# Performance work log

Measured on AMD Instinct MI355X. Metric: run time of the kernel, lower is better.

The kernel has to match this reference:

```python
import jax, jax.numpy as jnp
import numpy as np

B, L, H, O, N = 64, 2048, 128, 128, 256  # batch, window, num_states, num_actions, dynamics state dim


def setup_inputs() -> dict:
    key = jax.random.key(0)
    ks = jax.random.split(key, 12)
    # LRU-style stable init: |lambda| in (r_min, r_max)
    u1 = jax.random.uniform(ks[0], (N,))
    u2 = jax.random.uniform(ks[1], (N,))
    r_min, r_max = 0.4, 0.99
    nu_log = jnp.log(-0.5 * jnp.log(u1 * (r_max**2 - r_min**2) + r_min**2))
    theta_log = jnp.log(u2 * 2.0 * jnp.pi)
    lam_abs2 = jnp.exp(-2.0 * jnp.exp(nu_log))
    gamma_log = 0.5 * jnp.log(1.0 - lam_abs2)  # gamma normalization
    return {
        "state": jax.random.normal(ks[2], (B, H), jnp.float32),
        "dynamics_input_time_window": jax.random.normal(ks[3], (B, L, H), jnp.float32),
        "dynamics_disturbance_time_window": jax.random.normal(ks[4], (B, L, H), jnp.float32),
        "nu_log": nu_log.astype(jnp.float32),
        "theta_log": theta_log.astype(jnp.float32),
        "gamma_log": gamma_log.astype(jnp.float32),
        "B_re": jax.random.normal(ks[5], (N, H), jnp.float32) / np.sqrt(2 * H),
        "B_im": jax.random.normal(ks[6], (N, H), jnp.float32) / np.sqrt(2 * H),
        "C_re": jax.random.normal(ks[7], (O, N), jnp.float32) / np.sqrt(N),
        "C_im": jax.random.normal(ks[8], (O, N), jnp.float32) / np.sqrt(N),
        "D": jax.random.normal(ks[9], (O, H), jnp.float32) / np.sqrt(H),
    }


def _ssm_scan(u, nu_log, theta_log, gamma_log, B_re, B_im, C_re, C_im, D):
    # u: [B, L, H] real. Diagonal complex LRU: x_t = lam * x_{t-1} + gamma*B u_t; y = Re(C x) + D u
    lam = jnp.exp(-jnp.exp(nu_log) + 1j * jnp.exp(theta_log))           # [N]
    Bmat = (B_re + 1j * B_im) * jnp.exp(gamma_log)[:, None]              # [N, H]
    Bu = jnp.einsum("blh,nh->bln", u.astype(jnp.complex64), Bmat)       # [B, L, N]
    lam_seq = jnp.broadcast_to(lam, Bu.shape)

    def comb(e1, e2):
        a1, b1 = e1
        a2, b2 = e2
        return a1 * a2, a2 * b1 + b2

    _, x = jax.lax.associative_scan(comb, (lam_seq, Bu), axis=1)        # [B, L, N]
    y = jnp.einsum("bln,on->blo", x, C_re + 1j * C_im).real
    y = y + jnp.einsum("blh,oh->blo", u, D)
    return y


def reference(state, dynamics_input_time_window, dynamics_disturbance_time_window,
              nu_log, theta_log, gamma_log, B_re, B_im, C_re, C_im, D):
    # 3-dim branch of Actor.forward: run SSM over the disturbance window, take last step
    y = _ssm_scan(dynamics_disturbance_time_window, nu_log, theta_log, gamma_log,
                  B_re, B_im, C_re, C_im, D)                             # [B, L, O]
    action = y[:, -1, :]                                                 # [B, O]
    return action
```

## Files before the change

kernel.cpp:

```cpp
#include <hip/hip_runtime.h>
#include <hip/hip_bf16.h>

#define B_ 64
#define L_ 2048
#define H_ 128
#define O_ 128
#define N_ 256
#define TC_ 256
#define NCHUNK_ 8
#define NSTRIP_ 16

using f32x4 = __attribute__((ext_vector_type(4))) float;
using s16x8 = __attribute__((ext_vector_type(8))) short;
using i32x4 = __attribute__((ext_vector_type(4))) int;

__device__ __forceinline__ int pack_bf16(float a, float b) {
    return (int)((__float_as_uint(a) >> 16) | (__float_as_uint(b) & 0xffff0000u));
}

__global__ void prep_kernel(const float* __restrict__ nu_log, const float* __restrict__ theta_log,
                            const float* __restrict__ gamma_log, const float* __restrict__ B_re,
                            const float* __restrict__ B_im, unsigned short* __restrict__ B2T,
                            float2* __restrict__ lamj, float2* __restrict__ lam16t,
                            float2* __restrict__ lamC) {
    if (blockIdx.x < 64) {
        #pragma unroll
        for (int i = 0; i < 4; ++i) {
            int idx = blockIdx.x * 1024 + i * 256 + threadIdx.x;
            int col = idx >> 7;
            int h = idx & 127;
            int n = col & (N_ - 1);
            float g = expf(gamma_log[n]);
            float v = (col < N_ ? B_re[n * H_ + h] : B_im[n * H_ + h]) * g;
            unsigned ub = __float_as_uint(v);
            B2T[idx] = (unsigned short)((ub + 0x7fffu + ((ub >> 16) & 1u)) >> 16);
        }
    } else {
        int n = threadIdx.x;
        double lnr = -(double)expf(nu_log[n]);
        double th = (double)expf(theta_log[n]);
        double r = exp(lnr);
        double sn, cs;
        sincos(th, &sn, &cs);
        double lre = r * cs, lim = r * sn;
        double pre = 1.0, pim = 0.0;
        for (int k = 0; k < 16; ++k) {
            lamj[n * 16 + 15 - k] = make_float2((float)pre, (float)pim);
            double t1 = pre * lre - pim * lim;
            double t2 = pre * lim + pim * lre;
            pre = t1; pim = t2;
        }
        lam16t[n] = make_float2((float)pre, (float)pim);
        double wre = pre, wim = pim;
        for (int i = 0; i < 4; ++i) {
            double t1 = wre * wre - wim * wim;
            double t2 = 2.0 * wre * wim;
            wre = t1; wim = t2;
        }
        double are = 1.0, aim = 0.0;
        for (int cc = 7; cc >= 0; --cc) {
            lamC[cc * N_ + n] = make_float2((float)are, (float)aim);
            double t1 = are * wre - aim * wim;
            double t2 = are * wim + aim * wre;
            are = t1; aim = t2;
        }
    }
}

__global__ __launch_bounds__(256, 2)
void scan_kernel(const float* __restrict__ u, const unsigned short* __restrict__ B2T,
                 const float2* __restrict__ lamj, const float2* __restrict__ lam16t,
                 const float2* __restrict__ lamC, float* __restrict__ X) {
    const int b = blockIdx.x >> 3;
    const int c = blockIdx.x & 7;
    const int wave = (threadIdx.x >> 6) & 3;
    const int lane = threadIdx.x & 63;
    const int m = lane & 15;
    const int q = lane >> 4;

    s16x8 bf[4][2][4];
    float2 wl[4][4];
    float2 l16[4];

    #pragma unroll
    for (int p = 0; p < 4; ++p) {
        const int n = wave * 64 + p * 16 + m;
        #pragma unroll
        for (int part = 0; part < 2; ++part) {
            const unsigned short* rp = B2T + (size_t)(part * N_ + n) * H_ + q * 8;
            #pragma unroll
            for (int sl = 0; sl < 4; ++sl)
                bf[p][part][sl] = *(const s16x8*)(rp + sl * 32);
        }
        #pragma unroll
        for (int r = 0; r < 4; ++r) wl[p][r] = lamj[n * 16 + q * 4 + r];
        l16[p] = lam16t[n];
    }

    float2 zr[4], zi[4];
    #pragma unroll
    for (int p = 0; p < 4; ++p) {
        zr[p] = make_float2(0.f, 0.f);
        zi[p] = make_float2(0.f, 0.f);
    }

    const float* ub = u + ((size_t)b * L_ + (size_t)c * TC_) * H_;

    #pragma unroll 1
    for (int s = 0; s < NSTRIP_; ++s) {
        const float* up = ub + (s * 16 + m) * H_ + q * 8;
        float4 ua[8];
        #pragma unroll
        for (int sl = 0; sl < 4; ++sl) {
            ua[2 * sl]     = *(const float4*)(up + sl * 32);
            ua[2 * sl + 1] = *(const float4*)(up + sl * 32 + 4);
        }
        s16x8 afr[4];
        #pragma unroll
        for (int sl = 0; sl < 4; ++sl) {
            i32x4 w;
            w[0] = pack_bf16(ua[2 * sl].x, ua[2 * sl].y);
            w[1] = pack_bf16(ua[2 * sl].z, ua[2 * sl].w);
            w[2] = pack_bf16(ua[2 * sl + 1].x, ua[2 * sl + 1].y);
            w[3] = pack_bf16(ua[2 * sl + 1].z, ua[2 * sl + 1].w);
            afr[sl] = __builtin_bit_cast(s16x8, w);
        }
        #pragma unroll
        for (int p = 0; p < 4; ++p) {
            float2 a = zr[p];
            zr[p].x = l16[p].x * a.x - l16[p].y * a.y;
            zr[p].y = l16[p].x * a.y + l16[p].y * a.x;
            float2 bb = zi[p];
            zi[p].x = l16[p].x * bb.x - l16[p].y * bb.y;
            zi[p].y = l16[p].x * bb.y + l16[p].y * bb.x;
        }
        #pragma unroll
        for (int p = 0; p < 4; ++p) {
            f32x4 acc = {0.f, 0.f, 0.f, 0.f};
            #pragma unroll
            for (int sl = 0; sl < 4; ++sl)
                acc = __builtin_amdgcn_mfma_f32_16x16x32_bf16(afr[sl], bf[p][0][sl], acc, 0, 0, 0);
            #pragma unroll
            for (int r = 0; r < 4; ++r) {
                zr[p].x += wl[p][r].x * acc[r];
                zr[p].y += wl[p][r].y * acc[r];
            }
            f32x4 acc2 = {0.f, 0.f, 0.f, 0.f};
            #pragma unroll
            for (int sl = 0; sl < 4; ++sl)
                acc2 = __builtin_amdgcn_mfma_f32_16x16x32_bf16(afr[sl], bf[p][1][sl], acc2, 0, 0, 0);
            #pragma unroll
            for (int r = 0; r < 4; ++r) {
                zi[p].x += wl[p][r].x * acc2[r];
                zi[p].y += wl[p][r].y * acc2[r];
            }
        }
    }

    #pragma unroll
    for (int p = 0; p < 4; ++p) {
        zr[p].x += __shfl_xor(zr[p].x, 16); zr[p].x += __shfl_xor(zr[p].x, 32);
        zr[p].y += __shfl_xor(zr[p].y, 16); zr[p].y += __shfl_xor(zr[p].y, 32);
        zi[p].x += __shfl_xor(zi[p].x, 16); zi[p].x += __shfl_xor(zi[p].x, 32);
        zi[p].y += __shfl_xor(zi[p].y, 16); zi[p].y += __shfl_xor(zi[p].y, 32);
    }

    if (lane < 16) {
        #pragma unroll
        for (int p = 0; p < 4; ++p) {
            const int n = wave * 64 + p * 16 + m;
            float2 lc = lamC[c * N_ + n];
            float prr = lc.x * zr[p].x - lc.y * zr[p].y;
            float pri = lc.x * zr[p].y + lc.y * zr[p].x;
            float pir = lc.x * zi[p].x - lc.y * zi[p].y;
            float pii = lc.x * zi[p].y + lc.y * zi[p].x;
            atomicAdd(&X[(size_t)(b * N_ + n) * 2 + 0], prr - pii);
            atomicAdd(&X[(size_t)(b * N_ + n) * 2 + 1], pri + pir);
        }
    }
}

__global__ void out_kernel(const float* __restrict__ X, const float* __restrict__ C_re,
                           const float* __restrict__ C_im, const float* __restrict__ Dm,
                           const float* __restrict__ u, float* __restrict__ out) {
    __shared__ float xre[N_], xim[N_], ul[H_];
    const int b = blockIdx.x;
    const int t = threadIdx.x;
    xre[t] = X[(size_t)(b * N_ + t) * 2 + 0];
    xim[t] = X[(size_t)(b * N_ + t) * 2 + 1];
    if (t < H_) ul[t] = u[((size_t)b * L_ + (L_ - 1)) * H_ + t];
    __syncthreads();
    const int o = t >> 1;
    const int h = t & 1;
    const float* cre = C_re + o * N_ + h * 128;
    const float* cim = C_im + o * N_ + h * 128;
    const float* xr = xre + h * 128;
    const float* xi = xim + h * 128;
    float s = 0.f;
    #pragma unroll 4
    for (int n = 0; n < 128; ++n) s += cre[n] * xr[n] - cim[n] * xi[n];
    const float* dp = Dm + o * H_ + h * 64;
    const float* up = ul + h * 64;
    #pragma unroll 4
    for (int k = 0; k < 64; ++k) s += dp[k] * up[k];
    s += __shfl_xor(s, 1);
    if (h == 0) out[b * O_ + o] = s;
}

extern "C" void kernel_launch(void* const* d_in, const int* in_sizes, int n_in,
                              void* d_out, int out_size, void* d_ws, size_t ws_size,
                              hipStream_t stream) {
    const float* u         = (const float*)d_in[2];
    const float* nu_log    = (const float*)d_in[3];
    const float* theta_log = (const float*)d_in[4];
    const float* gamma_log = (const float*)d_in[5];
    const float* B_re      = (const float*)d_in[6];
    const float* B_im      = (const float*)d_in[7];
    const float* C_re      = (const float*)d_in[8];
    const float* C_im      = (const float*)d_in[9];
    const float* Dm        = (const float*)d_in[10];

    char* ws = (char*)d_ws;
    float*          X      = (float*)ws;
    unsigned short* B2T    = (unsigned short*)(ws + 131072);
    float2*         lamj   = (float2*)(ws + 262144);
    float2*         lam16t = (float2*)(ws + 294912);
    float2*         lamC   = (float2*)(ws + 296960);

    hipMemsetAsync(X, 0, (size_t)B_ * N_ * 2 * sizeof(float), stream);
    prep_kernel<<<65, 256, 0, stream>>>(nu_log, theta_log, gamma_log, B_re, B_im,
                                        B2T, lamj, lam16t, lamC);
    scan_kernel<<<B_ * NCHUNK_, 256, 0, stream>>>(u, B2T, lamj, lam16t, lamC, X);
    out_kernel<<<B_, 256, 0, stream>>>(X, C_re, C_im, Dm, u, (float*)d_out);
}
```

Baseline: 207.3 us.

## Recast last-step SSM as power-weighted GEMM over time with decay-based truncation

Since only the final state is needed, the chunked scan is replaced by a direct sum x_N = sum_t lam^(L-1-t) (B u_t). A precomputed bf16 table of lambda powers (real and imaginary rows) is multiplied against u over time with MFMA, and B is applied afterwards in fp32. Eigenvalue rows are sorted by decay rate so each 64-row tile can skip early time steps whose weight falls below exp(-35), cutting the u traffic for fast-decaying modes. This adds two prep kernels, a bf16 rounding of the power table, and per-element atomics in the epilogue.

```diff
diff --git a/kernel.cpp b/kernel.cpp
--- a/kernel.cpp
+++ b/kernel.cpp
@@ -1,14 +1,18 @@
 #include <hip/hip_runtime.h>
 #include <hip/hip_bf16.h>
+#include <math.h>
 
 #define B_ 64
 #define L_ 2048
 #define H_ 128
 #define O_ 128
 #define N_ 256
-#define TC_ 256
-#define NCHUNK_ 8
-#define NSTRIP_ 16
+
+#define BM_ 64
+#define BK_ 32
+#define KST_ 64
+#define NMT_ 8
+#define BROW_ 40
 
 using f32x4 = __attribute__((ext_vector_type(4))) float;
 using s16x8 = __attribute__((ext_vector_type(8))) short;
@@ -17,165 +21,197 @@
 __device__ __forceinline__ int pack_bf16(float a, float b) {
     return (int)((__float_as_uint(a) >> 16) | (__float_as_uint(b) & 0xffff0000u));
 }
-
-__global__ void prep_kernel(const float* __restrict__ nu_log, const float* __restrict__ theta_log,
-                            const float* __restrict__ gamma_log, const float* __restrict__ B_re,
-                            const float* __restrict__ B_im, unsigned short* __restrict__ B2T,
-                            float2* __restrict__ lamj, float2* __restrict__ lam16t,
-                            float2* __restrict__ lamC) {
-    if (blockIdx.x < 64) {
-        #pragma unroll
-        for (int i = 0; i < 4; ++i) {
-            int idx = blockIdx.x * 1024 + i * 256 + threadIdx.x;
-            int col = idx >> 7;
-            int h = idx & 127;
-            int n = col & (N_ - 1);
+__device__ __forceinline__ unsigned short bf16_rne(float v) {
+    unsigned u = __float_as_uint(v);
+    return (unsigned short)((u + 0x7fffu + ((u >> 16) & 1u)) >> 16);
+}
+
+__global__ void prep1_kernel(const float* __restrict__ nu_log, const float* __restrict__ gamma_log,
+                             const float* __restrict__ B_re, const float* __restrict__ B_im,
+                             float* __restrict__ X, float* __restrict__ Bgr, float* __restrict__ Bgi,
+                             int* __restrict__ perm, int* __restrict__ ksg) {
+    if (blockIdx.x == 0) {
+        __shared__ float nu_s[N_];
+        __shared__ int perm_s[N_];
+        const int n = threadIdx.x;
+        float nu = expf(nu_log[n]);
+        nu_s[n] = nu;
+        __syncthreads();
+        int rank = 0;
+        for (int j = 0; j < N_; ++j) {
+            float vj = nu_s[j];
+            rank += (vj < nu || (vj == nu && j < n)) ? 1 : 0;
+        }
+        perm_s[rank] = n;
+        __syncthreads();
+        perm[n] = perm_s[n];
+        if (n < NMT_) {
+            float nu0 = nu_s[perm_s[n * 32]];
+            float cutoff = 35.0f / nu0;
+            int kst = L_ - 1 - (int)cutoff;
+            if (kst < 0) kst = 0;
+            ksg[n] = kst >> 5;
+        }
+    } else {
+        const int i = (blockIdx.x - 1) * 256 + threadIdx.x;
+        #pragma unroll
+        for (int kk = 0; kk < 2; ++kk) {
+            int idx = i * 2 + kk;
+            int n = idx >> 7;
             float g = expf(gamma_log[n]);
-            float v = (col < N_ ? B_re[n * H_ + h] : B_im[n * H_ + h]) * g;
-            unsigned ub = __float_as_uint(v);
-            B2T[idx] = (unsigned short)((ub + 0x7fffu + ((ub >> 16) & 1u)) >> 16);
-        }
-    } else {
-        int n = threadIdx.x;
-        double lnr = -(double)expf(nu_log[n]);
-        double th = (double)expf(theta_log[n]);
-        double r = exp(lnr);
-        double sn, cs;
-        sincos(th, &sn, &cs);
-        double lre = r * cs, lim = r * sn;
-        double pre = 1.0, pim = 0.0;
-        for (int k = 0; k < 16; ++k) {
-            lamj[n * 16 + 15 - k] = make_float2((float)pre, (float)pim);
-            double t1 = pre * lre - pim * lim;
-            double t2 = pre * lim + pim * lre;
-            pre = t1; pim = t2;
-        }
-        lam16t[n] = make_float2((float)pre, (float)pim);
-        double wre = pre, wim = pim;
-        for (int i = 0; i < 4; ++i) {
-            double t1 = wre * wre - wim * wim;
-            double t2 = 2.0 * wre * wim;
-            wre = t1; wim = t2;
-        }
-        double are = 1.0, aim = 0.0;
-        for (int cc = 7; cc >= 0; --cc) {
-            lamC[cc * N_ + n] = make_float2((float)are, (float)aim);
-            double t1 = are * wre - aim * wim;
-            double t2 = are * wim + aim * wre;
-            are = t1; aim = t2;
-        }
-    }
-}
-
-__global__ __launch_bounds__(256, 2)
-void scan_kernel(const float* __restrict__ u, const unsigned short* __restrict__ B2T,
-                 const float2* __restrict__ lamj, const float2* __restrict__ lam16t,
-                 const float2* __restrict__ lamC, float* __restrict__ X) {
-    const int b = blockIdx.x >> 3;
-    const int c = blockIdx.x & 7;
-    const int wave = (threadIdx.x >> 6) & 3;
-    const int lane = threadIdx.x & 63;
-    const int m = lane & 15;
-    const int q = lane >> 4;
-
-    s16x8 bf[4][2][4];
-    float2 wl[4][4];
-    float2 l16[4];
-
+            Bgr[idx] = B_re[idx] * g;
+            Bgi[idx] = B_im[idx] * g;
+        }
+        X[i * 2] = 0.f;
+        X[i * 2 + 1] = 0.f;
+    }
+}
+
+__global__ void prep2_kernel(const float* __restrict__ nu_log, const float* __restrict__ theta_log,
+                             const int* __restrict__ perm, unsigned short* __restrict__ Lam) {
+    const int row = blockIdx.x;
+    const int rank = row >> 1, part = row & 1;
+    const int n = perm[rank];
+    const float nu = expf(nu_log[n]);
+    const double th = (double)expf(theta_log[n]);
+    const int t0 = threadIdx.x * 8;
+    union { unsigned short us[8]; s16x8 v; } w;
     #pragma unroll
-    for (int p = 0; p < 4; ++p) {
-        const int n = wave * 64 + p * 16 + m;
-        #pragma unroll
-        for (int part = 0; part < 2; ++part) {
-            const unsigned short* rp = B2T + (size_t)(part * N_ + n) * H_ + q * 8;
-            #pragma unroll
-            for (int sl = 0; sl < 4; ++sl)
-                bf[p][part][sl] = *(const s16x8*)(rp + sl * 32);
-        }
-        #pragma unroll
-        for (int r = 0; r < 4; ++r) wl[p][r] = lamj[n * 16 + q * 4 + r];
-        l16[p] = lam16t[n];
-    }
-
-    float2 zr[4], zi[4];
+    for (int j = 0; j < 8; ++j) {
+        int e = L_ - 1 - (t0 + j);
+        float mag = expf(-nu * (float)e);
+        double ang = (double)e * th;
+        ang -= floor(ang * (1.0 / 6.283185307179586)) * 6.283185307179586;
+        float s, c;
+        __sincosf((float)ang, &s, &c);
+        w.us[j] = bf16_rne(mag * (part ? s : c));
+    }
+    *(s16x8*)(Lam + (size_t)row * L_ + t0) = w.v;
+}
+
+__global__ __launch_bounds__(256, 4)
+void gemm_kernel(const float* __restrict__ u, const unsigned short* __restrict__ Lam,
+                 const float* __restrict__ Bgr, const float* __restrict__ Bgi,
+                 const int* __restrict__ perm, const int* __restrict__ ksg,
+                 float* __restrict__ X) {
+    const int bx = blockIdx.x;
+    const int mt = bx >> 7;
+    const int kc = (bx >> 6) & 1;
+    const int b  = bx & 63;
+    const int tid = threadIdx.x;
+    const int wave = tid >> 6, lane = tid & 63;
+    const int m16 = lane & 15, q = lane >> 4;
+
+    const int ks = ksg[mt];
+    const int S = KST_ - ks;
+    const int half = (S + 1) >> 1;
+    const int s0 = ks + kc * half;
+    const int s1 = (s0 + half < KST_) ? (s0 + half) : KST_;
+    if (s0 >= s1) return;
+
+    __shared__ unsigned short Asm[2][BM_ * BK_];
+    __shared__ unsigned short Bsm[2][H_ * BROW_];
+
+    const float* ub = u + (size_t)b * (L_ * H_);
+    const unsigned short* Ag = Lam + (size_t)(mt * BM_) * L_;
+
+    const int qs = tid & 3, rs = tid >> 2;
+    const int hs = tid & 127, tq = tid >> 7;
+    const float* ubt = ub + (size_t)tq * 16 * H_ + hs;
+    const unsigned short* Agt = Ag + (size_t)rs * L_ + qs * 8;
+    unsigned short* AsmW[2] = { &Asm[0][(qs * 64 + rs) * 8], &Asm[1][(qs * 64 + rs) * 8] };
+    unsigned short* BsmW[2] = { &Bsm[0][hs * BROW_ + tq * 16], &Bsm[1][hs * BROW_ + tq * 16] };
+
+    f32x4 acc[4][2];
     #pragma unroll
-    for (int p = 0; p < 4; ++p) {
-        zr[p] = make_float2(0.f, 0.f);
-        zi[p] = make_float2(0.f, 0.f);
-    }
-
-    const float* ub = u + ((size_t)b * L_ + (size_t)c * TC_) * H_;
-
-    #pragma unroll 1
-    for (int s = 0; s < NSTRIP_; ++s) {
-        const float* up = ub + (s * 16 + m) * H_ + q * 8;
-        float4 ua[8];
-        #pragma unroll
-        for (int sl = 0; sl < 4; ++sl) {
-            ua[2 * sl]     = *(const float4*)(up + sl * 32);
-            ua[2 * sl + 1] = *(const float4*)(up + sl * 32 + 4);
-        }
-        s16x8 afr[4];
-        #pragma unroll
-        for (int sl = 0; sl < 4; ++sl) {
-            i32x4 w;
-            w[0] = pack_bf16(ua[2 * sl].x, ua[2 * sl].y);
-            w[1] = pack_bf16(ua[2 * sl].z, ua[2 * sl].w);
-            w[2] = pack_bf16(ua[2 * sl + 1].x, ua[2 * sl + 1].y);
-            w[3] = pack_bf16(ua[2 * sl + 1].z, ua[2 * sl + 1].w);
-            afr[sl] = __builtin_bit_cast(s16x8, w);
-        }
-        #pragma unroll
-        for (int p = 0; p < 4; ++p) {
-            float2 a = zr[p];
-            zr[p].x = l16[p].x * a.x - l16[p].y * a.y;
-            zr[p].y = l16[p].x * a.y + l16[p].y * a.x;
-            float2 bb = zi[p];
-            zi[p].x = l16[p].x * bb.x - l16[p].y * bb.y;
-            zi[p].y = l16[p].x * bb.y + l16[p].y * bb.x;
-        }
-        #pragma unroll
-        for (int p = 0; p < 4; ++p) {
-            f32x4 acc = {0.f, 0.f, 0.f, 0.f};
-            #pragma unroll
-            for (int sl = 0; sl < 4; ++sl)
-                acc = __builtin_amdgcn_mfma_f32_16x16x32_bf16(afr[sl], bf[p][0][sl], acc, 0, 0, 0);
-            #pragma unroll
-            for (int r = 0; r < 4; ++r) {
-                zr[p].x += wl[p][r].x * acc[r];
-                zr[p].y += wl[p][r].y * acc[r];
+    for (int i = 0; i < 4; ++i)
+        #pragma unroll
+        for (int jn = 0; jn < 2; ++jn)
+            acc[i][jn] = (f32x4){0.f, 0.f, 0.f, 0.f};
+
+    {
+        s16x8 areg = *(const s16x8*)(Agt + (size_t)s0 * BK_);
+        float v[16];
+        const float* up = ubt + (size_t)s0 * BK_ * H_;
+        #pragma unroll
+        for (int j = 0; j < 16; ++j) v[j] = up[j * H_];
+        *(s16x8*)AsmW[0] = areg;
+        i32x4 w0, w1;
+        w0[0] = pack_bf16(v[0], v[1]);   w0[1] = pack_bf16(v[2], v[3]);
+        w0[2] = pack_bf16(v[4], v[5]);   w0[3] = pack_bf16(v[6], v[7]);
+        w1[0] = pack_bf16(v[8], v[9]);   w1[1] = pack_bf16(v[10], v[11]);
+        w1[2] = pack_bf16(v[12], v[13]); w1[3] = pack_bf16(v[14], v[15]);
+        *(i32x4*)BsmW[0] = w0;
+        *(i32x4*)(BsmW[0] + 8) = w1;
+    }
+    __syncthreads();
+
+    int cur = 0;
+    for (int kt = s0; kt < s1; ++kt) {
+        const int nxt = kt + 1;
+        const bool pf = (nxt < s1);
+        s16x8 areg;
+        float v[16];
+        if (pf) {
+            areg = *(const s16x8*)(Agt + (size_t)nxt * BK_);
+            const float* up = ubt + (size_t)nxt * BK_ * H_;
+            #pragma unroll
+            for (int j = 0; j < 16; ++j) v[j] = up[j * H_];
+        }
+        const unsigned short* As = Asm[cur];
+        const unsigned short* Bs = Bsm[cur];
+        s16x8 afr[4], bfr[2];
+        #pragma unroll
+        for (int i = 0; i < 4; ++i)
+            afr[i] = *(const s16x8*)(As + (q * 64 + i * 16 + m16) * 8);
+        #pragma unroll
+        for (int jn = 0; jn < 2; ++jn)
+            bfr[jn] = *(const s16x8*)(Bs + (wave * 32 + jn * 16 + m16) * BROW_ + q * 8);
+        #pragma unroll
+        for (int i = 0; i < 4; ++i)
+            #pragma unroll
+            for (int jn = 0; jn < 2; ++jn)
+                acc[i][jn] = __builtin_amdgcn_mfma_f32_16x16x32_bf16(afr[i], bfr[jn], acc[i][jn], 0, 0, 0);
+        if (pf) {
+            *(s16x8*)AsmW[cur ^ 1] = areg;
+            i32x4 w0, w1;
+            w0[0] = pack_bf16(v[0], v[1]);   w0[1] = pack_bf16(v[2], v[3]);
+            w0[2] = pack_bf16(v[4], v[5]);   w0[3] = pack_bf16(v[6], v[7]);
+            w1[0] = pack_bf16(v[8], v[9]);   w1[1] = pack_bf16(v[10], v[11]);
+            w1[2] = pack_bf16(v[12], v[13]); w1[3] = pack_bf16(v[14], v[15]);
+            *(i32x4*)BsmW[cur ^ 1] = w0;
+            *(i32x4*)(BsmW[cur ^ 1] + 8) = w1;
+        }
+        __syncthreads();
+        cur ^= 1;
+    }
+
+    #pragma unroll
+    for (int i = 0; i < 4; ++i) {
+        #pragma unroll
+        for (int r = 0; r < 4; ++r) {
+            const int row = mt * BM_ + i * 16 + q * 4 + r;
+            const int nid = perm[row >> 1];
+            const int part = r & 1;
+            float xre = 0.f, xim = 0.f;
+            #pragma unroll
+            for (int jn = 0; jn < 2; ++jn) {
+                const int h = wave * 32 + jn * 16 + m16;
+                const float g = acc[i][jn][r];
+                const float br = Bgr[nid * H_ + h];
+                const float bi = Bgi[nid * H_ + h];
+                if (part == 0) { xre += br * g; xim += bi * g; }
+                else           { xre -= bi * g; xim += br * g; }
             }
-            f32x4 acc2 = {0.f, 0.f, 0.f, 0.f};
-            #pragma unroll
-            for (int sl = 0; sl < 4; ++sl)
-                acc2 = __builtin_amdgcn_mfma_f32_16x16x32_bf16(afr[sl], bf[p][1][sl], acc2, 0, 0, 0);
-            #pragma unroll
-            for (int r = 0; r < 4; ++r) {
-                zi[p].x += wl[p][r].x * acc2[r];
-                zi[p].y += wl[p][r].y * acc2[r];
+            #pragma unroll
+            for (int d = 1; d < 16; d <<= 1) {
+                xre += __shfl_xor(xre, d);
+                xim += __shfl_xor(xim, d);
             }
-        }
-    }
-
-    #pragma unroll
-    for (int p = 0; p < 4; ++p) {
-        zr[p].x += __shfl_xor(zr[p].x, 16); zr[p].x += __shfl_xor(zr[p].x, 32);
-        zr[p].y += __shfl_xor(zr[p].y, 16); zr[p].y += __shfl_xor(zr[p].y, 32);
-        zi[p].x += __shfl_xor(zi[p].x, 16); zi[p].x += __shfl_xor(zi[p].x, 32);
-        zi[p].y += __shfl_xor(zi[p].y, 16); zi[p].y += __shfl_xor(zi[p].y, 32);
-    }
-
-    if (lane < 16) {
-        #pragma unroll
-        for (int p = 0; p < 4; ++p) {
-            const int n = wave * 64 + p * 16 + m;
-            float2 lc = lamC[c * N_ + n];
-            float prr = lc.x * zr[p].x - lc.y * zr[p].y;
-            float pri = lc.x * zr[p].y + lc.y * zr[p].x;
-            float pir = lc.x * zi[p].x - lc.y * zi[p].y;
-            float pii = lc.x * zi[p].y + lc.y * zi[p].x;
-            atomicAdd(&X[(size_t)(b * N_ + n) * 2 + 0], prr - pii);
-            atomicAdd(&X[(size_t)(b * N_ + n) * 2 + 1], pri + pir);
+            if (m16 == 0) {
+                atomicAdd(&X[(b * N_ + nid) * 2 + 0], xre);
+                atomicAdd(&X[(b * N_ + nid) * 2 + 1], xim);
+            }
         }
     }
 }
@@ -221,15 +257,15 @@
     const float* Dm        = (const float*)d_in[10];
 
     char* ws = (char*)d_ws;
-    float*          X      = (float*)ws;
-    unsigned short* B2T    = (unsigned short*)(ws + 131072);
-    float2*         lamj   = (float2*)(ws + 262144);
-    float2*         lam16t = (float2*)(ws + 294912);
-    float2*         lamC   = (float2*)(ws + 296960);
-
-    hipMemsetAsync(X, 0, (size_t)B_ * N_ * 2 * sizeof(float), stream);
-    prep_kernel<<<65, 256, 0, stream>>>(nu_log, theta_log, gamma_log, B_re, B_im,
-                                        B2T, lamj, lam16t, lamC);
-    scan_kernel<<<B_ * NCHUNK_, 256, 0, stream>>>(u, B2T, lamj, lam16t, lamC, X);
+    float*          X    = (float*)ws;
+    unsigned short* Lam  = (unsigned short*)(ws + 131072);
+    float*          Bgr  = (float*)(ws + 2228224);
+    float*          Bgi  = (float*)(ws + 2359296);
+    int*            perm = (int*)(ws + 2490368);
+    int*            ksg  = (int*)(ws + 2491392);
+
+    prep1_kernel<<<65, 256, 0, stream>>>(nu_log, gamma_log, B_re, B_im, X, Bgr, Bgi, perm, ksg);
+    prep2_kernel<<<512, 256, 0, stream>>>(nu_log, theta_log, perm, Lam);
+    gemm_kernel<<<1024, 256, 0, stream>>>(u, Lam, Bgr, Bgi, perm, ksg, X);
     out_kernel<<<B_, 256, 0, stream>>>(X, C_re, C_im, Dm, u, (float*)d_out);
 }
```

After: 200.8 us. 1.03x faster.
